# Kernel tuning notes

Hardware: AMD Instinct MI355X
Metric: run time of the kernel (lower is better)

## Reference

```python
import jax, jax.numpy as jnp
import numpy as np

NUM_ROT = 8
OUT_CH = 128
IN_CH = 128
KSIZE = 3


def _resample(filt, angle):
    """Rotate a (O, I, k, k) filter bank by `angle` via bilinear resampling,
    matching F.affine_grid/F.grid_sample with align_corners=True, zero padding."""
    k = filt.shape[-1]
    c, s = jnp.cos(angle), jnp.sin(angle)
    lin = jnp.linspace(-1.0, 1.0, k)
    gy, gx = jnp.meshgrid(lin, lin, indexing='ij')  # (k, k) output coords
    # theta = [[c, -s, 0], [s, c, 0]] applied to (x, y, 1)
    xs = c * gx - s * gy
    ys = s * gx + c * gy
    ix = (xs + 1.0) * 0.5 * (k - 1)  # normalized -> pixel coords
    iy = (ys + 1.0) * 0.5 * (k - 1)
    x0f, y0f = jnp.floor(ix), jnp.floor(iy)
    x0, y0 = x0f.astype(jnp.int32), y0f.astype(jnp.int32)
    wx, wy = ix - x0f, iy - y0f

    def tap(yi, xi, w):
        valid = ((yi >= 0) & (yi < k) & (xi >= 0) & (xi < k)).astype(filt.dtype)
        yc = jnp.clip(yi, 0, k - 1)
        xc = jnp.clip(xi, 0, k - 1)
        return filt[:, :, yc, xc] * (valid * w)  # (O, I, k, k)

    return (tap(y0, x0, (1 - wy) * (1 - wx)) + tap(y0, x0 + 1, (1 - wy) * wx)
            + tap(y0 + 1, x0, wy * (1 - wx)) + tap(y0 + 1, x0 + 1, wy * wx))


def setup_inputs() -> dict:
    key = jax.random.key(0)
    k1, k2, k3 = jax.random.split(key, 3)
    x = jax.random.normal(k1, (16, IN_CH, 128, 128), jnp.float32)
    # base_conv.weight: (out_channels * num_rotations, in_channels, k, k)
    weight = jax.random.normal(k2, (OUT_CH * NUM_ROT, IN_CH, KSIZE, KSIZE), jnp.float32) * 0.05
    rot_alpha = jax.random.normal(k3, (NUM_ROT,), jnp.float32) * 0.1 + 1.0
    return {"x": x, "weight": weight, "rot_alpha": rot_alpha}


def reference(x, weight, rot_alpha):
    R, O, K = NUM_ROT, OUT_CH, KSIZE
    # weight.view(O, R, I, K, K)[:, i] per rotation -> (R, O, I, K, K)
    w_r = weight.reshape(O, R, -1, K, K).transpose(1, 0, 2, 3, 4)
    angles = rot_alpha * (jnp.pi / 4) * jnp.arange(R, dtype=jnp.float32)
    rot_w = jax.vmap(_resample)(w_r, angles)  # (R, O, I, K, K)
    filters = rot_w.reshape(R * O, -1, K, K)
    # one conv with all rotated filter banks instead of R separate convs
    y = jax.lax.conv_general_dilated(
        x, filters, window_strides=(1, 1),
        padding=[(K // 2, K // 2), (K // 2, K // 2)],
        dimension_numbers=('NCHW', 'OIHW', 'NCHW'))  # (B, R*O, H, W)
    B, _, H, W = y.shape
    return y.reshape(B, R, O, H, W).max(axis=1)  # max over rotations
```

## Files before the change

kernel.cpp:

```cpp
#include <hip/hip_runtime.h>

typedef short short8 __attribute__((ext_vector_type(8)));
typedef float f32x4 __attribute__((ext_vector_type(4)));

#define XP_BYTES (16ull * 130 * 130 * 128 * 2)

static __device__ __forceinline__ unsigned short f2bf(float f) {
  unsigned u = __float_as_uint(f);
  u += 0x7FFFu + ((u >> 16) & 1u);
  return (unsigned short)(u >> 16);
}

static __device__ __forceinline__ void gload16(const void* g, void* l) {
  __builtin_amdgcn_global_load_lds(
      (const __attribute__((address_space(1))) void*)g,
      (__attribute__((address_space(3))) void*)l, 16, 0, 0);
}

static __device__ __forceinline__ float wtap(const float* f, int yi, int xi) {
  bool valid = (yi >= 0) & (yi < 3) & (xi >= 0) & (xi < 3);
  int yc = min(max(yi, 0), 2), xc = min(max(xi, 0), 2);
  return valid ? f[yc * 3 + xc] : 0.f;
}

__global__ __launch_bounds__(256) void wprep_kernel(
    const float* __restrict__ w, const float* __restrict__ rot_alpha,
    unsigned short* __restrict__ w2) {
  int gid = blockIdx.x * 256 + threadIdx.x;
  int ic = gid & 127;
  int nr = gid >> 7;
  int r = nr & 7;
  const float* wf = w + (size_t)nr * (128 * 9) + (size_t)ic * 9;
  float f[9];
#pragma unroll
  for (int q = 0; q < 9; ++q) f[q] = wf[q];
  float ang = rot_alpha[r] * 0.78539816339744830962f * (float)r;
  float sth, cth;
  sincosf(ang, &sth, &cth);
#pragma unroll
  for (int j = 0; j < 3; ++j) {
#pragma unroll
    for (int i = 0; i < 3; ++i) {
      float gy = (float)(j - 1), gx = (float)(i - 1);
      float xs = cth * gx - sth * gy;
      float ys = sth * gx + cth * gy;
      float ix = xs + 1.0f, iy = ys + 1.0f;
      float x0f = floorf(ix), y0f = floorf(iy);
      int x0 = (int)x0f, y0 = (int)y0f;
      float wx = ix - x0f, wy = iy - y0f;
      float acc = wtap(f, y0, x0) * (1.f - wy) * (1.f - wx)
                + wtap(f, y0, x0 + 1) * (1.f - wy) * wx
                + wtap(f, y0 + 1, x0) * wy * (1.f - wx)
                + wtap(f, y0 + 1, x0 + 1) * wy * wx;
      w2[(size_t)nr * 1152 + (size_t)(j * 3 + i) * 128 + ic] = f2bf(acc);
    }
  }
}

__global__ __launch_bounds__(256) void xprep_kernel(
    const float* __restrict__ x, unsigned short* __restrict__ xp) {
  const int yy = blockIdx.x;
  const int b = blockIdx.y;
  const int t = threadIdx.x;
  const size_t rowbase = ((size_t)b * 130 + yy) * (130 * 128);
  if (yy == 0 || yy == 129) {
    uint4 z = {0u, 0u, 0u, 0u};
    for (int i = t; i < 2080; i += 256)
      ((uint4*)(xp + rowbase))[i] = z;
    return;
  }
  const int y = yy - 1;
  __shared__ float lt[32][129];
  if (t < 32) {
    uint4 z = {0u, 0u, 0u, 0u};
    int xx = (t < 16) ? 0 : 129;
    int cc = (t & 15) * 8;
    *(uint4*)(xp + rowbase + (size_t)xx * 128 + cc) = z;
  }
  for (int c0 = 0; c0 < 128; c0 += 32) {
#pragma unroll
    for (int i = 0; i < 16; ++i) {
      int idx = i * 256 + t;
      int c = idx >> 7, wq = idx & 127;
      lt[c][wq] = x[(((size_t)b * 128 + c0 + c) * 128 + y) * 128 + wq];
    }
    __syncthreads();
#pragma unroll
    for (int i = 0; i < 2; ++i) {
      int u = i * 256 + t;
      int xx = u >> 2, cp = (u & 3) * 8;
      unsigned short v[8];
#pragma unroll
      for (int q = 0; q < 8; ++q) v[q] = f2bf(lt[cp + q][xx]);
      *(uint4*)(xp + rowbase + (size_t)(xx + 1) * 128 + c0 + cp) = *(uint4*)v;
    }
    __syncthreads();
  }
}

__global__ __launch_bounds__(256, 2) void conv_kernel(
    const unsigned short* __restrict__ xp,
    const unsigned short* __restrict__ w2,
    float* __restrict__ out) {
  __shared__ unsigned short lds[32768];

  const int tid = threadIdx.x;
  const int lane = tid & 63;
  const int wv = tid >> 6;
  const int wr = wv >> 1;
  const int wc = wv & 1;

  const int bid = blockIdx.x;
  const int wg = (bid & 7) * 2048 + (bid >> 3);
  const int mblk = wg >> 3;
  const int nblk = wg & 7;
  const int b = mblk >> 7;
  const int y = mblk & 127;

  const int r0 = tid >> 2;
  const int s0 = tid & 3;
  const int g0 = s0 ^ ((r0 >> 1) & 3);

  const unsigned short* xpt =
      xp + (size_t)(b * 130 + y) * 130 * 128 + r0 * 128 + g0 * 8;
  const unsigned short* wpt =
      w2 + (size_t)nblk * 128 * 1152 + (size_t)r0 * 1152 + g0 * 8;

  const int l15 = lane & 15;
  const int lhi = lane >> 4;
  const int sa = (lhi ^ ((l15 >> 1) & 3)) * 8;

  const int aRd = wr * 2048 + l15 * 32 + sa;
  const int bRd = 16384 + wc * 2048 + l15 * 32 + sa;

  f32x4 acc[4][4];
#pragma unroll
  for (int mf = 0; mf < 4; ++mf)
#pragma unroll
    for (int nf = 0; nf < 4; ++nf) acc[mf][nf] = (f32x4){0.f, 0.f, 0.f, 0.f};

#define STAGE_A(BUF, HALF, KK, DY, DX, CH)                                    \
  gload16(xpt + ((DY) * 130 + (HALF) * 64 + (DX)) * 128 + (CH) * 64 + (KK) * 32, \
          lds + (BUF) * 8192 + (KK) * 4096 + (HALF) * 2048 + wv * 512)
#define STAGE_B(BUF, HALF, KK, TAP, CH)                                       \
  gload16(wpt + (size_t)(HALF) * 64 * 1152 + (TAP) * 128 + (CH) * 64 + (KK) * 32, \
          lds + 16384 + (BUF) * 8192 + (KK) * 4096 + (HALF) * 2048 + wv * 512)

#define VMW(n) asm volatile("s_waitcnt vmcnt(" #n ")" ::: "memory")
#define LGKM0 asm volatile("s_waitcnt lgkmcnt(0)" ::: "memory")
#define SCH0 __builtin_amdgcn_sched_barrier(0)

#define STAGE_HALF(BUF, KK, T)                                                \
  {                                                                           \
    const int tp_ = (T) >> 1, c_ = (T) & 1;                                   \
    const int dy_ = tp_ / 3, dx_ = tp_ - dy_ * 3;                             \
    STAGE_A(BUF, 0, KK, dy_, dx_, c_);                                        \
    STAGE_A(BUF, 1, KK, dy_, dx_, c_);                                        \
    STAGE_B(BUF, 0, KK, tp_, c_);                                             \
    STAGE_B(BUF, 1, KK, tp_, c_);                                             \
  }

#define PHASE(BUF, KK, STG, VMX)                                              \
  {                                                                           \
    const unsigned short* pA_ = lds + (BUF) * 8192 + (KK) * 4096 + aRd;       \
    const unsigned short* pB_ = lds + (BUF) * 8192 + (KK) * 4096 + bRd;       \
    short8 af[4], bf[4];                                                      \
    _Pragma("unroll") for (int q = 0; q < 4; ++q)                             \
        af[q] = *(const short8*)(pA_ + q * 512);                              \
    _Pragma("unroll") for (int n = 0; n < 4; ++n)                             \
        bf[n] = *(const short8*)(pB_ + n * 512);                              \
    STG;                                                                      \
    SCH0;                                                                     \
    __builtin_amdgcn_s_barrier();                                             \
    LGKM0;                                                                    \
    __builtin_amdgcn_s_setprio(1);                                            \
    _Pragma("unroll") for (int q = 0; q < 4; ++q)                             \
        _Pragma("unroll") for (int n = 0; n < 4; ++n)                         \
            acc[q][n] = __builtin_amdgcn_mfma_f32_16x16x32_bf16(              \
                af[q], bf[n], acc[q][n], 0, 0, 0);                            \
    __builtin_amdgcn_s_setprio(0);                                            \
    VMX;                                                                      \
    __builtin_amdgcn_s_barrier();                                             \
  }

  STAGE_HALF(0, 0, 0);
  STAGE_HALF(0, 1, 0);
  STAGE_HALF(1, 0, 1);
  VMW(8);
  SCH0;
  __builtin_amdgcn_s_barrier();

#pragma unroll 1
  for (int kt = 0; kt < 16; ++kt) {
    const int buf_ = kt & 1;
    PHASE(buf_, 0, STAGE_HALF(buf_ ^ 1, 1, kt + 1), VMW(8));
    PHASE(buf_, 1, STAGE_HALF(buf_, 0, kt + 2), VMW(8));
  }
  PHASE(0, 0, STAGE_HALF(1, 1, 17), VMW(8));
  PHASE(0, 1, , VMW(4));
  PHASE(1, 0, , VMW(0));
  PHASE(1, 1, , VMW(0));

#undef PHASE
#undef STAGE_HALF
#undef STAGE_A
#undef STAGE_B

  float* lE = (float*)lds;
#pragma unroll
  for (int mf = 0; mf < 4; ++mf)
#pragma unroll
    for (int nf = 0; nf < 4; ++nf)
#pragma unroll
      for (int j = 0; j < 4; ++j) {
        float v = acc[mf][nf][j];
        v = fmaxf(v, __shfl_xor(v, 1, 64));
        v = fmaxf(v, __shfl_xor(v, 2, 64));
        v = fmaxf(v, __shfl_xor(v, 4, 64));
        if ((lane & 7) == 0) {
          int pix = wr * 64 + mf * 16 + lhi * 4 + j;
          int ol = wc * 8 + nf * 2 + ((lane >> 3) & 1);
          lE[pix * 17 + ol] = v;
        }
      }
  __syncthreads();
  const size_t obase = ((size_t)(b * 128 + nblk * 16) * 128 + y) * 128;
#pragma unroll
  for (int i = 0; i < 8; ++i) {
    int idx = i * 256 + tid;
    int ol = idx >> 7;
    int xx = idx & 127;
    out[obase + (size_t)ol * 16384 + xx] = lE[xx * 17 + ol];
  }
}

extern "C" void kernel_launch(void* const* d_in, const int* in_sizes, int n_in,
                              void* d_out, int out_size, void* d_ws, size_t ws_size,
                              hipStream_t stream) {
  const float* x = (const float*)d_in[0];
  const float* w = (const float*)d_in[1];
  const float* ra = (const float*)d_in[2];
  float* out = (float*)d_out;
  unsigned short* xp = (unsigned short*)d_ws;
  unsigned short* w2 = (unsigned short*)((char*)d_ws + XP_BYTES);

  hipLaunchKernelGGL(wprep_kernel, dim3(512), dim3(256), 0, stream, w, ra, w2);
  hipLaunchKernelGGL(xprep_kernel, dim3(130, 16), dim3(256), 0, stream, x, xp);
  hipLaunchKernelGGL(conv_kernel, dim3(16384), dim3(256), 0, stream, xp, w2, out);
}
```

Measured before the change: 812.1 us.

## Load weight fragments directly to registers, halving LDS and restructuring pipeline

The B (weight) operand is now loaded from global memory straight into registers, double-buffered across two register sets, instead of staging through LDS. The LDS buffer shrinks to half, holding only the input tile with two full K-tile buffers. The main loop is rewritten to process a full tap/channel step per iteration, with a full vmcnt(0) wait and one barrier per step. This removes LDS traffic and barriers for weights, but adds register pressure, uncoalesced per-lane global loads, and coarser synchronization that may expose memory latency.

```diff
diff --git a/kernel.cpp b/kernel.cpp
--- a/kernel.cpp
+++ b/kernel.cpp
@@ -102,7 +102,7 @@
     const unsigned short* __restrict__ xp,
     const unsigned short* __restrict__ w2,
     float* __restrict__ out) {
-  __shared__ unsigned short lds[32768];
+  __shared__ unsigned short lds[16384];
 
   const int tid = threadIdx.x;
   const int lane = tid & 63;
@@ -123,15 +123,14 @@
 
   const unsigned short* xpt =
       xp + (size_t)(b * 130 + y) * 130 * 128 + r0 * 128 + g0 * 8;
-  const unsigned short* wpt =
-      w2 + (size_t)nblk * 128 * 1152 + (size_t)r0 * 1152 + g0 * 8;
 
   const int l15 = lane & 15;
   const int lhi = lane >> 4;
   const int sa = (lhi ^ ((l15 >> 1) & 3)) * 8;
-
   const int aRd = wr * 2048 + l15 * 32 + sa;
-  const int bRd = 16384 + wc * 2048 + l15 * 32 + sa;
+
+  const unsigned short* wb =
+      w2 + (size_t)(nblk * 128 + wc * 64 + l15) * 1152 + lhi * 8;
 
   f32x4 acc[4][4];
 #pragma unroll
@@ -139,72 +138,81 @@
 #pragma unroll
     for (int nf = 0; nf < 4; ++nf) acc[mf][nf] = (f32x4){0.f, 0.f, 0.f, 0.f};
 
-#define STAGE_A(BUF, HALF, KK, DY, DX, CH)                                    \
-  gload16(xpt + ((DY) * 130 + (HALF) * 64 + (DX)) * 128 + (CH) * 64 + (KK) * 32, \
-          lds + (BUF) * 8192 + (KK) * 4096 + (HALF) * 2048 + wv * 512)
-#define STAGE_B(BUF, HALF, KK, TAP, CH)                                       \
-  gload16(wpt + (size_t)(HALF) * 64 * 1152 + (TAP) * 128 + (CH) * 64 + (KK) * 32, \
-          lds + 16384 + (BUF) * 8192 + (KK) * 4096 + (HALF) * 2048 + wv * 512)
-
-#define VMW(n) asm volatile("s_waitcnt vmcnt(" #n ")" ::: "memory")
-#define LGKM0 asm volatile("s_waitcnt lgkmcnt(0)" ::: "memory")
-#define SCH0 __builtin_amdgcn_sched_barrier(0)
-
-#define STAGE_HALF(BUF, KK, T)                                                \
+#define STAGE_T(BUF, T)                                                       \
   {                                                                           \
     const int tp_ = (T) >> 1, c_ = (T) & 1;                                   \
     const int dy_ = tp_ / 3, dx_ = tp_ - dy_ * 3;                             \
-    STAGE_A(BUF, 0, KK, dy_, dx_, c_);                                        \
-    STAGE_A(BUF, 1, KK, dy_, dx_, c_);                                        \
-    STAGE_B(BUF, 0, KK, tp_, c_);                                             \
-    STAGE_B(BUF, 1, KK, tp_, c_);                                             \
-  }
-
-#define PHASE(BUF, KK, STG, VMX)                                              \
+    _Pragma("unroll") for (int kk_ = 0; kk_ < 2; ++kk_)                       \
+        _Pragma("unroll") for (int hf_ = 0; hf_ < 2; ++hf_)                   \
+            gload16(xpt + ((size_t)dy_ * 130 + hf_ * 64 + dx_) * 128 +        \
+                        c_ * 64 + kk_ * 32,                                   \
+                    lds + (BUF) * 8192 + kk_ * 4096 + hf_ * 2048 + wv * 512); \
+  }
+
+#define B_LOAD(DST, T)                                                        \
   {                                                                           \
-    const unsigned short* pA_ = lds + (BUF) * 8192 + (KK) * 4096 + aRd;       \
-    const unsigned short* pB_ = lds + (BUF) * 8192 + (KK) * 4096 + bRd;       \
-    short8 af[4], bf[4];                                                      \
+    const int tp_ = (T) >> 1, c_ = (T) & 1;                                   \
+    const unsigned short* wb_ = wb + tp_ * 128 + c_ * 64;                     \
+    _Pragma("unroll") for (int kk_ = 0; kk_ < 2; ++kk_)                       \
+        _Pragma("unroll") for (int nf_ = 0; nf_ < 4; ++nf_)                   \
+            DST[kk_ * 4 + nf_] =                                              \
+                *(const short8*)(wb_ + nf_ * 18432 + kk_ * 32);               \
+  }
+
+#define COMPUTE(BUF, BREG)                                                    \
+  {                                                                           \
+    const unsigned short* pA_ = lds + (BUF) * 8192 + aRd;                     \
+    short8 af[8];                                                             \
     _Pragma("unroll") for (int q = 0; q < 4; ++q)                             \
         af[q] = *(const short8*)(pA_ + q * 512);                              \
-    _Pragma("unroll") for (int n = 0; n < 4; ++n)                             \
-        bf[n] = *(const short8*)(pB_ + n * 512);                              \
-    STG;                                                                      \
-    SCH0;                                                                     \
-    __builtin_amdgcn_s_barrier();                                             \
-    LGKM0;                                                                    \
+    _Pragma("unroll") for (int q = 0; q < 4; ++q)                             \
+        af[4 + q] = *(const short8*)(pA_ + 4096 + q * 512);                   \
     __builtin_amdgcn_s_setprio(1);                                            \
     _Pragma("unroll") for (int q = 0; q < 4; ++q)                             \
         _Pragma("unroll") for (int n = 0; n < 4; ++n)                         \
             acc[q][n] = __builtin_amdgcn_mfma_f32_16x16x32_bf16(              \
-                af[q], bf[n], acc[q][n], 0, 0, 0);                            \
+                af[q], BREG[n], acc[q][n], 0, 0, 0);                          \
+    _Pragma("unroll") for (int q = 0; q < 4; ++q)                             \
+        _Pragma("unroll") for (int n = 0; n < 4; ++n)                         \
+            acc[q][n] = __builtin_amdgcn_mfma_f32_16x16x32_bf16(              \
+                af[4 + q], BREG[4 + n], acc[q][n], 0, 0, 0);                  \
     __builtin_amdgcn_s_setprio(0);                                            \
-    VMX;                                                                      \
-    __builtin_amdgcn_s_barrier();                                             \
-  }
-
-  STAGE_HALF(0, 0, 0);
-  STAGE_HALF(0, 1, 0);
-  STAGE_HALF(1, 0, 1);
-  VMW(8);
-  SCH0;
+  }
+
+#define VMW0 asm volatile("s_waitcnt vmcnt(0)" ::: "memory")
+#define SCH0 __builtin_amdgcn_sched_barrier(0)
+
+  short8 b0[8], b1[8];
+
+  B_LOAD(b0, 0);
+  STAGE_T(0, 0);
+  VMW0;
   __builtin_amdgcn_s_barrier();
 
 #pragma unroll 1
-  for (int kt = 0; kt < 16; ++kt) {
-    const int buf_ = kt & 1;
-    PHASE(buf_, 0, STAGE_HALF(buf_ ^ 1, 1, kt + 1), VMW(8));
-    PHASE(buf_, 1, STAGE_HALF(buf_, 0, kt + 2), VMW(8));
-  }
-  PHASE(0, 0, STAGE_HALF(1, 1, 17), VMW(8));
-  PHASE(0, 1, , VMW(4));
-  PHASE(1, 0, , VMW(0));
-  PHASE(1, 1, , VMW(0));
-
-#undef PHASE
-#undef STAGE_HALF
-#undef STAGE_A
-#undef STAGE_B
+  for (int i = 0; i < 9; ++i) {
+    const int te = 2 * i, to = te + 1;
+    B_LOAD(b1, to);
+    STAGE_T(1, to);
+    SCH0;
+    COMPUTE(0, b0);
+    VMW0;
+    __builtin_amdgcn_s_barrier();
+    if (i < 8) {
+      B_LOAD(b0, te + 2);
+      STAGE_T(0, te + 2);
+    }
+    SCH0;
+    COMPUTE(1, b1);
+    VMW0;
+    __builtin_amdgcn_s_barrier();
+  }
+
+#undef VMW0
+#undef SCH0
+#undef COMPUTE
+#undef B_LOAD
+#undef STAGE_T
 
   float* lE = (float*)lds;
 #pragma unroll
```

Result: slower. 1.360 ms (+67.5%).

## Switch conv GEMM to three-slot ring pipeline with smaller LDS for higher occupancy

Applied to the files above, without the earlier changes.

Replaces the double-buffered two-half-phase pipeline with a three-slot ring of 32-wide K chunks. Each step prefetches two chunks ahead and uses one barrier per step. LDS drops from 64KB to 48KB and launch bounds rise to 3 blocks per CU, which should hide more memory latency through occupancy. The tradeoffs are more barriers per unit of K work, less prefetch depth in bytes, and extra register pressure from the higher occupancy target.

```diff
diff --git a/kernel.cpp b/kernel.cpp
--- a/kernel.cpp
+++ b/kernel.cpp
@@ -98,11 +98,11 @@
   }
 }
 
-__global__ __launch_bounds__(256, 2) void conv_kernel(
+__global__ __launch_bounds__(256, 3) void conv_kernel(
     const unsigned short* __restrict__ xp,
     const unsigned short* __restrict__ w2,
     float* __restrict__ out) {
-  __shared__ unsigned short lds[32768];
+  __shared__ unsigned short lds[24576];
 
   const int tid = threadIdx.x;
   const int lane = tid & 63;
@@ -129,9 +129,8 @@
   const int l15 = lane & 15;
   const int lhi = lane >> 4;
   const int sa = (lhi ^ ((l15 >> 1) & 3)) * 8;
-
   const int aRd = wr * 2048 + l15 * 32 + sa;
-  const int bRd = 16384 + wc * 2048 + l15 * 32 + sa;
+  const int bRd = 12288 + wc * 2048 + l15 * 32 + sa;
 
   f32x4 acc[4][4];
 #pragma unroll
@@ -139,72 +138,62 @@
 #pragma unroll
     for (int nf = 0; nf < 4; ++nf) acc[mf][nf] = (f32x4){0.f, 0.f, 0.f, 0.f};
 
-#define STAGE_A(BUF, HALF, KK, DY, DX, CH)                                    \
-  gload16(xpt + ((DY) * 130 + (HALF) * 64 + (DX)) * 128 + (CH) * 64 + (KK) * 32, \
-          lds + (BUF) * 8192 + (KK) * 4096 + (HALF) * 2048 + wv * 512)
-#define STAGE_B(BUF, HALF, KK, TAP, CH)                                       \
-  gload16(wpt + (size_t)(HALF) * 64 * 1152 + (TAP) * 128 + (CH) * 64 + (KK) * 32, \
-          lds + 16384 + (BUF) * 8192 + (KK) * 4096 + (HALF) * 2048 + wv * 512)
-
-#define VMW(n) asm volatile("s_waitcnt vmcnt(" #n ")" ::: "memory")
-#define LGKM0 asm volatile("s_waitcnt lgkmcnt(0)" ::: "memory")
+#define STAGE_T(P, T)                                                         \
+  {                                                                           \
+    const int tp_ = (T) >> 2, cq_ = (T) & 3;                                  \
+    const int dy_ = tp_ / 3, dx_ = tp_ - dy_ * 3;                             \
+    _Pragma("unroll") for (int hf_ = 0; hf_ < 2; ++hf_) {                     \
+      gload16(xpt + ((size_t)dy_ * 130 + hf_ * 64 + dx_) * 128 + cq_ * 32,    \
+              lds + (P) * 4096 + hf_ * 2048 + wv * 512);                      \
+      gload16(wpt + (size_t)hf_ * 64 * 1152 + tp_ * 128 + cq_ * 32,           \
+              lds + 12288 + (P) * 4096 + hf_ * 2048 + wv * 512);              \
+    }                                                                         \
+  }
+
+#define VMW4 asm volatile("s_waitcnt vmcnt(4)" ::: "memory")
+#define VMW0 asm volatile("s_waitcnt vmcnt(0)" ::: "memory")
 #define SCH0 __builtin_amdgcn_sched_barrier(0)
 
-#define STAGE_HALF(BUF, KK, T)                                                \
+#define BODY(P, PN2, T)                                                       \
   {                                                                           \
-    const int tp_ = (T) >> 1, c_ = (T) & 1;                                   \
-    const int dy_ = tp_ / 3, dx_ = tp_ - dy_ * 3;                             \
-    STAGE_A(BUF, 0, KK, dy_, dx_, c_);                                        \
-    STAGE_A(BUF, 1, KK, dy_, dx_, c_);                                        \
-    STAGE_B(BUF, 0, KK, tp_, c_);                                             \
-    STAGE_B(BUF, 1, KK, tp_, c_);                                             \
-  }
-
-#define PHASE(BUF, KK, STG, VMX)                                              \
-  {                                                                           \
-    const unsigned short* pA_ = lds + (BUF) * 8192 + (KK) * 4096 + aRd;       \
-    const unsigned short* pB_ = lds + (BUF) * 8192 + (KK) * 4096 + bRd;       \
+    if ((T) + 2 < 36) STAGE_T(PN2, (T) + 2);                                  \
+    const unsigned short* pA_ = lds + (P) * 4096 + aRd;                       \
+    const unsigned short* pB_ = lds + (P) * 4096 + bRd;                       \
     short8 af[4], bf[4];                                                      \
     _Pragma("unroll") for (int q = 0; q < 4; ++q)                             \
         af[q] = *(const short8*)(pA_ + q * 512);                              \
     _Pragma("unroll") for (int n = 0; n < 4; ++n)                             \
         bf[n] = *(const short8*)(pB_ + n * 512);                              \
-    STG;                                                                      \
-    SCH0;                                                                     \
-    __builtin_amdgcn_s_barrier();                                             \
-    LGKM0;                                                                    \
     __builtin_amdgcn_s_setprio(1);                                            \
     _Pragma("unroll") for (int q = 0; q < 4; ++q)                             \
         _Pragma("unroll") for (int n = 0; n < 4; ++n)                         \
             acc[q][n] = __builtin_amdgcn_mfma_f32_16x16x32_bf16(              \
                 af[q], bf[n], acc[q][n], 0, 0, 0);                            \
     __builtin_amdgcn_s_setprio(0);                                            \
-    VMX;                                                                      \
+    SCH0;                                                                     \
+    if ((T) < 34) { VMW4; } else { VMW0; }                                    \
     __builtin_amdgcn_s_barrier();                                             \
   }
 
-  STAGE_HALF(0, 0, 0);
-  STAGE_HALF(0, 1, 0);
-  STAGE_HALF(1, 0, 1);
-  VMW(8);
+  STAGE_T(0, 0);
+  STAGE_T(1, 1);
+  VMW4;
   SCH0;
   __builtin_amdgcn_s_barrier();
 
 #pragma unroll 1
-  for (int kt = 0; kt < 16; ++kt) {
-    const int buf_ = kt & 1;
-    PHASE(buf_, 0, STAGE_HALF(buf_ ^ 1, 1, kt + 1), VMW(8));
-    PHASE(buf_, 1, STAGE_HALF(buf_, 0, kt + 2), VMW(8));
-  }
-  PHASE(0, 0, STAGE_HALF(1, 1, 17), VMW(8));
-  PHASE(0, 1, , VMW(4));
-  PHASE(1, 0, , VMW(0));
-  PHASE(1, 1, , VMW(0));
-
-#undef PHASE
-#undef STAGE_HALF
-#undef STAGE_A
-#undef STAGE_B
+  for (int j = 0; j < 12; ++j) {
+    const int t0 = j * 3;
+    BODY(0, 2, t0);
+    BODY(1, 0, t0 + 1);
+    BODY(2, 1, t0 + 2);
+  }
+
+#undef BODY
+#undef STAGE_T
+#undef VMW4
+#undef VMW0
+#undef SCH0
 
   float* lE = (float*)lds;
 #pragma unroll
```

Result: faster. 723.3 us (median of 2 runs) (-10.9%).
